# Kernel optimization log

Hardware: AMD Instinct MI355X
Metric: run time of the kernel (lower is better)

The kernel has to match this reference:

```python
import jax, jax.numpy as jnp
import numpy as np

H, D, BLK, R = 12, 64, 64, 3  # heads, size_per_head, block size, rand blocks
NEG = -1e9


def setup_inputs() -> dict:
    key = jax.random.key(0)
    ks = jax.random.split(key, 6)
    B, S, W = 2, 4096, H * D
    M = S // BLK
    return {
        "from_tensor": jax.random.normal(ks[0], (B, S, W), jnp.float32),
        "to_tensor": jax.random.normal(ks[1], (B, S, W), jnp.float32),
        "Wq": jax.random.normal(ks[2], (W, H * D), jnp.float32) * 0.02,
        "bq": jnp.zeros((H * D,), jnp.float32),
        "Wk": jax.random.normal(ks[3], (W, H * D), jnp.float32) * 0.02,
        "bk": jnp.zeros((H * D,), jnp.float32),
        "Wv": jax.random.normal(ks[4], (W, H * D), jnp.float32) * 0.02,
        "bv": jnp.zeros((H * D,), jnp.float32),
        "to_mask": jnp.ones((B, S), jnp.int32),
        "rand_attn": jax.random.randint(ks[5], (H, M - 2, R), 0, M - 2, jnp.int32),
    }


def _bigbird_block_sparse(from_tensor, to_tensor, Wq, bq, Wk, bk, Wv, bv, to_mask, rand_attn):
    B, S, _ = from_tensor.shape
    M = S // BLK
    scale = 1.0 / np.sqrt(D).astype(np.float32)

    # QKV projections -> [B,H,S,D]
    q = (from_tensor @ Wq + bq).reshape(B, S, H, D).transpose(0, 2, 1, 3)
    k = (to_tensor @ Wk + bk).reshape(B, S, H, D).transpose(0, 2, 1, 3)
    v = (to_tensor @ Wv + bv).reshape(B, S, H, D).transpose(0, 2, 1, 3)

    bq_ = q.reshape(B, H, M, BLK, D)
    bk_ = k.reshape(B, H, M, BLK, D)
    bv_ = v.reshape(B, H, M, BLK, D)

    tm = to_mask.astype(q.dtype)          # [B,S]
    bm = tm.reshape(B, M, BLK)            # [B,M,BLK]

    # gather random key/value blocks per head: [B,H,M-2,R*BLK,D]
    ha = jnp.arange(H)[:, None, None]
    gk = bk_[:, ha, rand_attn].reshape(B, H, M - 2, R * BLK, D)
    gv = bv_[:, ha, rand_attn].reshape(B, H, M - 2, R * BLK, D)
    gm = bm[:, rand_attn].reshape(B, H, M - 2, R * BLK)

    def full_row(qblk):  # first/last query blocks attend to everything
        s = jnp.einsum('bhqd,bhkd->bhqk', qblk, k) * scale + (1 - tm)[:, None, None, :] * NEG
        return jnp.einsum('bhqk,bhkd->bhqd', jax.nn.softmax(s, -1), v)

    def sparse_row(qblk, k_cat, v_cat, m_cat):  # [B,H,BLK,D] x [B,H,L,D]
        s = jnp.einsum('bhqd,bhkd->bhqk', qblk, k_cat) * scale + (1 - m_cat)[:, :, None, :] * NEG
        return jnp.einsum('bhqk,bhkd->bhqd', jax.nn.softmax(s, -1), v_cat)

    c_first = full_row(bq_[:, :, 0])
    c_last = full_row(bq_[:, :, M - 1])

    # second row: blocks [0,1,2,last] + rand
    k2 = jnp.concatenate([bk_[:, :, 0], bk_[:, :, 1], bk_[:, :, 2], bk_[:, :, M - 1], gk[:, :, 0]], axis=2)
    v2 = jnp.concatenate([bv_[:, :, 0], bv_[:, :, 1], bv_[:, :, 2], bv_[:, :, M - 1], gv[:, :, 0]], axis=2)
    m2s = jnp.concatenate([bm[:, 0], bm[:, 1], bm[:, 2], bm[:, M - 1]], axis=-1)
    m2 = jnp.concatenate([jnp.broadcast_to(m2s[:, None], (B, H, 4 * BLK)), gm[:, :, 0]], axis=-1)
    c_second = sparse_row(bq_[:, :, 1], k2, v2, m2)

    # second-to-last row: blocks [0,M-3,M-2,M-1] + rand
    k3 = jnp.concatenate([bk_[:, :, 0], bk_[:, :, M - 3], bk_[:, :, M - 2], bk_[:, :, M - 1], gk[:, :, M - 3]], axis=2)
    v3 = jnp.concatenate([bv_[:, :, 0], bv_[:, :, M - 3], bv_[:, :, M - 2], bv_[:, :, M - 1], gv[:, :, M - 3]], axis=2)
    m3s = jnp.concatenate([bm[:, 0], bm[:, M - 3], bm[:, M - 2], bm[:, M - 1]], axis=-1)
    m3 = jnp.concatenate([jnp.broadcast_to(m3s[:, None], (B, H, 4 * BLK)), gm[:, :, M - 3]], axis=-1)
    c_secondlast = sparse_row(bq_[:, :, M - 2], k3, v3, m3)

    # middle rows 2..M-3: band(prev,self,next) + rand + global first/last blocks
    L = M - 4
    band_k = jnp.concatenate([bk_[:, :, 1:M - 3], bk_[:, :, 2:M - 2], bk_[:, :, 3:M - 1]], axis=3)  # [B,H,L,3BLK,D]
    band_v = jnp.concatenate([bv_[:, :, 1:M - 3], bv_[:, :, 2:M - 2], bv_[:, :, 3:M - 1]], axis=3)
    band_m = jnp.concatenate([bm[:, 1:M - 3], bm[:, 2:M - 2], bm[:, 3:M - 1]], axis=-1)  # [B,L,3BLK]

    k_mid = jnp.concatenate([
        band_k, gk[:, :, 1:M - 3],
        jnp.broadcast_to(bk_[:, :, 0:1], (B, H, L, BLK, D)),
        jnp.broadcast_to(bk_[:, :, M - 1:M], (B, H, L, BLK, D))], axis=3)
    v_mid = jnp.concatenate([
        band_v, gv[:, :, 1:M - 3],
        jnp.broadcast_to(bv_[:, :, 0:1], (B, H, L, BLK, D)),
        jnp.broadcast_to(bv_[:, :, M - 1:M], (B, H, L, BLK, D))], axis=3)
    m_mid = jnp.concatenate([
        jnp.broadcast_to(band_m[:, None], (B, H, L, 3 * BLK)),
        gm[:, :, 1:M - 3],
        jnp.broadcast_to(bm[:, None, None, 0], (B, H, L, BLK)),
        jnp.broadcast_to(bm[:, None, None, M - 1], (B, H, L, BLK))], axis=-1)

    s_mid = jnp.einsum('bhlqd,bhlkd->bhlqk', bq_[:, :, 2:M - 2], k_mid) * scale
    s_mid = s_mid + (1 - m_mid)[:, :, :, None, :] * NEG
    c_mid = jnp.einsum('bhlqk,bhlkd->bhlqd', jax.nn.softmax(s_mid, -1), v_mid)

    ctx = jnp.concatenate([
        c_first[:, :, None], c_second[:, :, None], c_mid,
        c_secondlast[:, :, None], c_last[:, :, None]], axis=2)  # [B,H,M,BLK,D]
    return ctx.reshape(B, H, S, D).transpose(0, 2, 1, 3)  # [B,S,H,D]


def reference(from_tensor, to_tensor, Wq, bq, Wk, bk, Wv, bv, to_mask, rand_attn):
    return _bigbird_block_sparse(from_tensor, to_tensor, Wq, bq, Wk, bk, Wv, bv, to_mask, rand_attn)
```

## Files before the change

### kernel.cpp

```cpp
#include <hip/hip_runtime.h>

typedef __attribute__((ext_vector_type(4))) float f32x4;
typedef __attribute__((ext_vector_type(8))) __bf16 bf16x8;
typedef __attribute__((ext_vector_type(8))) unsigned short u16x8;
typedef __attribute__((ext_vector_type(4))) unsigned short u16x4;
typedef __attribute__((ext_vector_type(2))) unsigned int u32x2;

#define LOG2E 1.4426950408889634f

__device__ __forceinline__ unsigned short f2bf(float f) {
  unsigned u = __builtin_bit_cast(unsigned, f);
  u += 0x7fffu + ((u >> 16) & 1u);
  return (unsigned short)(u >> 16);
}

__device__ __forceinline__ unsigned cvtpk(float lo, float hi) {
  unsigned r;
  asm("v_cvt_pk_bf16_f32 %0, %1, %2" : "=v"(r) : "v"(lo), "v"(hi));
  return r;
}

__device__ __forceinline__ f32x4 mfma16(bf16x8 a, bf16x8 b, f32x4 c) {
  return __builtin_amdgcn_mfma_f32_16x16x32_bf16(a, b, c, 0, 0, 0);
}

__device__ __forceinline__ void gload_lds16(const void* g, void* l) {
  __builtin_amdgcn_global_load_lds(
      (const __attribute__((address_space(1))) void*)g,
      (__attribute__((address_space(3))) void*)l, 16, 0, 0);
}

#define NQK 6291456
#define NX 6291456
#define NW 589824

__global__ __launch_bounds__(256) void prep_kernel(
    const float* __restrict__ Wq, const float* __restrict__ Wk,
    const float* __restrict__ Wv, const float* __restrict__ from_t,
    const float* __restrict__ to_t, unsigned short* __restrict__ Wt,
    unsigned short* __restrict__ xb) {
  __shared__ float tile[64][65];
  const int bid = blockIdx.x;
  const int t = threadIdx.x;
  if (bid < 432) {
    const int z = bid / 144, rest = bid % 144;
    const float* __restrict__ src = (z == 0) ? Wq : (z == 1) ? Wk : Wv;
    unsigned short* __restrict__ dst = Wt + (size_t)z * NW;
    const int k0 = (rest / 12) * 64, n0 = (rest % 12) * 64;
    const int r = t >> 4, c4 = (t & 15) * 4;
#pragma unroll
    for (int p = 0; p < 4; ++p) {
      int rr = r + p * 16;
      f32x4 v = *(const f32x4*)(src + (size_t)(k0 + rr) * 768 + n0 + c4);
#pragma unroll
      for (int j = 0; j < 4; ++j) tile[rr][c4 + j] = v[j];
    }
    __syncthreads();
#pragma unroll
    for (int p = 0; p < 4; ++p) {
      int rn = r + p * 16;
      u16x4 o;
#pragma unroll
      for (int j = 0; j < 4; ++j) o[j] = f2bf(tile[c4 + j][rn]);
      *(u16x4*)(dst + (size_t)(n0 + rn) * 768 + k0 + c4) = o;
    }
  } else {
    const int idx = bid - 432;
    const int y = idx / 3072, xi = idx % 3072;
    const float* __restrict__ src = y ? to_t : from_t;
    unsigned short* __restrict__ dst = xb + (size_t)y * NX;
    const size_t i = ((size_t)xi * 256 + t) * 8;
    f32x4 a = *(const f32x4*)(src + i);
    f32x4 b = *(const f32x4*)(src + i + 4);
    u16x8 o;
#pragma unroll
    for (int j = 0; j < 4; ++j) { o[j] = f2bf(a[j]); o[j + 4] = f2bf(b[j]); }
    *(u16x8*)(dst + i) = o;
  }
}

__global__ __launch_bounds__(256) void qkv_gemm_kernel(
    const unsigned short* __restrict__ Xb, const unsigned short* __restrict__ Wt,
    const float* __restrict__ bq, const float* __restrict__ bk,
    const float* __restrict__ bv, unsigned short* __restrict__ qkvQK,
    unsigned short* __restrict__ vt, int zoff, int cpx) {
  __shared__ unsigned short A_lds[2][8192];
  __shared__ unsigned short B_lds[2][8192];
  const int bid0 = blockIdx.x;
  const int bid = (bid0 & 7) * cpx + (bid0 >> 3);
  const int z = zoff + bid / 384;
  const int rem = bid % 384;
  const int bm = rem / 6, bn = rem % 6;
  const unsigned short* __restrict__ X = Xb + (z ? (size_t)NX : 0);
  const unsigned short* __restrict__ Wz = Wt + (size_t)z * NW;
  const float* __restrict__ bias = (z == 0) ? bq : (z == 1) ? bk : bv;
  const int t = threadIdx.x, lane = t & 63, w = t >> 6;
  const int wm = (w >> 1) * 64, wn = (w & 1) * 64;
  const int l15 = lane & 15, cc = lane >> 4;

  f32x4 acc[4][4];
#pragma unroll
  for (int i = 0; i < 4; ++i)
#pragma unroll
    for (int j = 0; j < 4; ++j) acc[i][j] = (f32x4){0.f, 0.f, 0.f, 0.f};

  const unsigned short* Abase = X + (size_t)bm * 128 * 768;
  const unsigned short* Bbase = Wz + (size_t)bn * 128 * 768;

  auto STAGE = [&](int ks, int bufi) {
#pragma unroll
    for (int p = 0; p < 4; ++p) {
      int wb = p * 4 + w;
      int ch = wb * 64 + lane;
      int r = ch >> 3, sl = ch & 7;
      int g = sl ^ (r & 7);
      gload_lds16(Abase + (size_t)r * 768 + ks * 64 + g * 8,
                  &A_lds[bufi][wb * 512]);
      gload_lds16(Bbase + (size_t)r * 768 + ks * 64 + g * 8,
                  &B_lds[bufi][wb * 512]);
    }
  };

  STAGE(0, 0);

  for (int ks = 0; ks < 12; ++ks) {
    const int cur = ks & 1;
    if (ks < 11) {
      STAGE(ks + 1, cur ^ 1);
      asm volatile("s_waitcnt vmcnt(8)" ::: "memory");
    } else {
      asm volatile("s_waitcnt vmcnt(0)" ::: "memory");
    }
    __builtin_amdgcn_s_barrier();
    __builtin_amdgcn_sched_barrier(0);

    bf16x8 af[4][2], bfr[4][2];
#pragma unroll
    for (int mi = 0; mi < 4; ++mi) {
      int row = wm + mi * 16 + l15;
      const char* rp = (const char*)A_lds[cur] + row * 128;
#pragma unroll
      for (int kk = 0; kk < 2; ++kk)
        af[mi][kk] = *(const bf16x8*)(rp + (((cc + 4 * kk) ^ (row & 7)) << 4));
    }
#pragma unroll
    for (int ni = 0; ni < 4; ++ni) {
      int row = wn + ni * 16 + l15;
      const char* rp = (const char*)B_lds[cur] + row * 128;
#pragma unroll
      for (int kk = 0; kk < 2; ++kk)
        bfr[ni][kk] = *(const bf16x8*)(rp + (((cc + 4 * kk) ^ (row & 7)) << 4));
    }
#pragma unroll
    for (int kk = 0; kk < 2; ++kk)
#pragma unroll
      for (int mi = 0; mi < 4; ++mi)
#pragma unroll
        for (int ni = 0; ni < 4; ++ni)
          acc[mi][ni] = mfma16(af[mi][kk], bfr[ni][kk], acc[mi][ni]);
    asm volatile("s_waitcnt lgkmcnt(0)" ::: "memory");
    __builtin_amdgcn_s_barrier();
  }

  if (z < 2) {
    const float qscale = (z == 0) ? 0.125f * LOG2E : 1.0f;
    unsigned short* __restrict__ dst = qkvQK + (size_t)z * NQK;
#pragma unroll
    for (int ni = 0; ni < 4; ++ni) {
      int gn = bn * 128 + wn + ni * 16 + l15;
      float bv_ = bias[gn];
      int hh = gn >> 6, dd = gn & 63;
#pragma unroll
      for (int mi = 0; mi < 4; ++mi) {
#pragma unroll
        for (int r = 0; r < 4; ++r) {
          int gm = bm * 128 + wm + mi * 16 + cc * 4 + r;
          int bb = gm >> 12, s = gm & 4095;
          float val = (acc[mi][ni][r] + bv_) * qscale;
          dst[((((size_t)bb * 12 + hh) * 4096 + s) * 64) + dd] = f2bf(val);
        }
      }
    }
  } else {
#pragma unroll
    for (int ni = 0; ni < 4; ++ni) {
      int gn = bn * 128 + wn + ni * 16 + l15;
      float bv_ = bias[gn];
      int hh = gn >> 6, dd = gn & 63;
#pragma unroll
      for (int mi = 0; mi < 4; ++mi) {
        int gm0 = bm * 128 + wm + mi * 16 + cc * 4;
        int bb = gm0 >> 12, s0 = gm0 & 4095;
        u16x4 o;
#pragma unroll
        for (int r = 0; r < 4; ++r) o[r] = f2bf(acc[mi][ni][r] + bv_);
        *(u16x4*)(vt + ((size_t)(bb * 12 + hh) * 64 + dd) * 4096 + s0) = o;
      }
    }
  }
}

__global__ __launch_bounds__(256) void attn_kernel(
    const unsigned short* __restrict__ qkvQK, const unsigned short* __restrict__ vt,
    const int* __restrict__ to_mask, const int* __restrict__ rand_attn,
    float* __restrict__ out, float* __restrict__ part_o,
    float* __restrict__ part_ml) {
  __shared__ unsigned short K_lds[4][4096];
  __shared__ unsigned short VT_lds[4][4096];
  __shared__ unsigned short P_lds[4][1024];
  __shared__ float penal[8][64];
  __shared__ int blist[8];

  const int bid0 = blockIdx.x;
  const int bid = (bid0 & 7) * 234 + (bid0 >> 3);
  const int bh = bid / 78, r78 = bid % 78;
  const int h = bh % 12, b = bh / 12;
  const int t = threadIdx.x, lane = t & 63, w = t >> 6;
  const int l15 = lane & 15, cc = lane >> 4;

  int m, nblk, chunk = 0;
  bool full;
  if (r78 < 62) {
    full = false;
    m = r78 + 1;
    nblk = (m == 1 || m == 62) ? 7 : 8;
    if (t == 0) {
      const int* rp = rand_attn + ((size_t)h * 62 + (m - 1)) * 3;
      if (m == 1) {
        blist[0] = 0; blist[1] = 1; blist[2] = 2; blist[3] = 63;
        blist[4] = rp[0]; blist[5] = rp[1]; blist[6] = rp[2];
      } else if (m == 62) {
        blist[0] = 0; blist[1] = 61; blist[2] = 62; blist[3] = 63;
        blist[4] = rp[0]; blist[5] = rp[1]; blist[6] = rp[2];
      } else {
        blist[0] = m - 1; blist[1] = m; blist[2] = m + 1;
        blist[3] = rp[0]; blist[4] = rp[1]; blist[5] = rp[2];
        blist[6] = 0; blist[7] = 63;
      }
    }
  } else {
    full = true;
    int fr = r78 - 62;
    chunk = fr & 7;
    m = (fr >> 3) ? 63 : 0;
    nblk = 8;
    if (t < 8) blist[t] = chunk * 8 + t;
  }

  const unsigned short* qp = qkvQK + (((size_t)b * 12 + h) * 4096 + m * 64) * 64;
  const unsigned short* kp = qkvQK + NQK + (((size_t)b * 12 + h) * 4096) * 64;
  const unsigned short* vtp = vt + (((size_t)b * 12 + h) * 64) * 4096;

  int loff[2];
  const unsigned short *kpl[2], *vpl[2];
#pragma unroll
  for (int p = 0; p < 2; ++p) {
    int wb = p * 4 + w;
    int ch = wb * 64 + lane;
    int rr = ch >> 3;
    int g = (ch & 7) ^ (rr & 7);
    loff[p] = wb * 512;
    kpl[p] = kp + rr * 64 + g * 8;
    vpl[p] = vtp + rr * 4096 + g * 8;
  }

  bf16x8 aq[2];
  {
    int qrow = w * 16 + l15;
    aq[0] = *(const bf16x8*)(qp + qrow * 64 + cc * 8);
    aq[1] = *(const bf16x8*)(qp + qrow * 64 + 32 + cc * 8);
  }

  float m_run = -INFINITY, l_run = 0.f;
  f32x4 o_acc[4];
#pragma unroll
  for (int dg = 0; dg < 4; ++dg) o_acc[dg] = (f32x4){0.f, 0.f, 0.f, 0.f};

  char* pw = (char*)P_lds[w];
  const int swz = (l15 & 7) << 4;

  auto STAGE = [&](int kb, int bufi) {
    const size_t ko = (size_t)kb * 4096;
    const size_t vo = (size_t)kb * 64;
    gload_lds16(kpl[0] + ko, &K_lds[bufi][loff[0]]);
    gload_lds16(kpl[1] + ko, &K_lds[bufi][loff[1]]);
    gload_lds16(vpl[0] + vo, &VT_lds[bufi][loff[0]]);
    gload_lds16(vpl[1] + vo, &VT_lds[bufi][loff[1]]);
  };

  __syncthreads();

  {
    int ib = w;
#pragma unroll
    for (int pp = 0; pp < 2; ++pp, ib += 4)
      if (ib < nblk)
        penal[ib][lane] =
            (1.0f - (float)to_mask[(size_t)b * 4096 + blist[ib] * 64 + lane]) *
            (-1e9f * LOG2E);
  }
  STAGE(blist[0], 0);
  STAGE(blist[1], 1);
  asm volatile("s_waitcnt lgkmcnt(0)" ::: "memory");
  __builtin_amdgcn_s_barrier();

  for (int ib = 0; ib < nblk; ++ib) {
    const int bi = ib & 3;
    if (ib + 2 < nblk) {
      STAGE(blist[ib + 2], (ib + 2) & 3);
      asm volatile("s_waitcnt vmcnt(8)" ::: "memory");
    } else if (ib + 1 < nblk) {
      asm volatile("s_waitcnt vmcnt(4)" ::: "memory");
    } else {
      asm volatile("s_waitcnt vmcnt(0)" ::: "memory");
    }
    __builtin_amdgcn_s_barrier();
    __builtin_amdgcn_sched_barrier(0);

    float sm[4][4];
    const char* kbase = (const char*)K_lds[bi];
#pragma unroll
    for (int kg = 0; kg < 4; ++kg) {
      int krow = kg * 16 + l15;
      const char* rp = kbase + krow * 128;
      int sz = (krow & 7) << 4;
      bf16x8 k0 = *(const bf16x8*)(rp + ((cc << 4) ^ sz));
      bf16x8 k1 = *(const bf16x8*)(rp + (((cc + 4) << 4) ^ sz));
      f32x4 zz = (f32x4){0.f, 0.f, 0.f, 0.f};
      zz = mfma16(k0, aq[0], zz);
      zz = mfma16(k1, aq[1], zz);
      f32x4 pen = *(const f32x4*)(&penal[ib][kg * 16 + cc * 4]);
#pragma unroll
      for (int r = 0; r < 4; ++r) sm[kg][r] = zz[r] + pen[r];
    }

    float mk[4];
#pragma unroll
    for (int kg = 0; kg < 4; ++kg)
      mk[kg] = fmaxf(fmaxf(sm[kg][0], sm[kg][1]), fmaxf(sm[kg][2], sm[kg][3]));
    float mx = fmaxf(fmaxf(mk[0], mk[1]), fmaxf(mk[2], mk[3]));
    mx = fmaxf(mx, __shfl_xor(mx, 16, 64));
    mx = fmaxf(mx, __shfl_xor(mx, 32, 64));

    if (!__all(mx - m_run <= 8.0f)) {
      float mn = fmaxf(m_run, mx);
      float fac = exp2f(m_run - mn);
      m_run = mn;
      l_run *= fac;
      float fr_[4];
#pragma unroll
      for (int r = 0; r < 4; ++r) fr_[r] = __shfl(fac, cc * 4 + r, 64);
#pragma unroll
      for (int dg = 0; dg < 4; ++dg)
#pragma unroll
        for (int r = 0; r < 4; ++r) o_acc[dg][r] *= fr_[r];
    }

    float rs = 0.f;
#pragma unroll
    for (int kg = 0; kg < 4; ++kg) {
      float p0 = exp2f(sm[kg][0] - m_run), p1 = exp2f(sm[kg][1] - m_run);
      float p2 = exp2f(sm[kg][2] - m_run), p3 = exp2f(sm[kg][3] - m_run);
      rs += (p0 + p1) + (p2 + p3);
      u32x2 wv;
      wv[0] = cvtpk(p0, p1);
      wv[1] = cvtpk(p2, p3);
      *(u32x2*)(pw + l15 * 128 + ((kg * 32 + cc * 8) ^ swz)) = wv;
    }
    rs += __shfl_xor(rs, 16, 64);
    rs += __shfl_xor(rs, 32, 64);
    l_run += rs;

    __builtin_amdgcn_wave_barrier();
    bf16x8 ap0 = *(const bf16x8*)(pw + l15 * 128 + ((cc << 4) ^ swz));
    bf16x8 ap1 = *(const bf16x8*)(pw + l15 * 128 + (((cc + 4) << 4) ^ swz));

    const char* vbase = (const char*)VT_lds[bi];
#pragma unroll
    for (int dg = 0; dg < 4; ++dg) {
      int drow = dg * 16 + l15;
      const char* vb = vbase + drow * 128;
      int sz = (drow & 7) << 4;
      bf16x8 v0 = *(const bf16x8*)(vb + ((cc << 4) ^ sz));
      bf16x8 v1 = *(const bf16x8*)(vb + (((cc + 4) << 4) ^ sz));
      o_acc[dg] = mfma16(ap0, v0, o_acc[dg]);
      o_acc[dg] = mfma16(ap1, v1, o_acc[dg]);
    }
  }

  if (!full) {
    float inv[4];
#pragma unroll
    for (int r = 0; r < 4; ++r) inv[r] = 1.0f / __shfl(l_run, cc * 4 + r, 64);
#pragma unroll
    for (int r = 0; r < 4; ++r) {
      int s = m * 64 + w * 16 + cc * 4 + r;
#pragma unroll
      for (int dg = 0; dg < 4; ++dg) {
        int d = dg * 16 + l15;
        out[(((size_t)b * 4096 + s) * 12 + h) * 64 + d] = o_acc[dg][r] * inv[r];
      }
    }
  } else {
    const int row = (b * 12 + h) * 2 + (m ? 1 : 0);
    float* po = part_o + (((size_t)row * 8 + chunk) * 64) * 64;
    float* pml = part_ml + ((size_t)row * 8 + chunk) * 128;
#pragma unroll
    for (int r = 0; r < 4; ++r) {
      int q = w * 16 + cc * 4 + r;
#pragma unroll
      for (int dg = 0; dg < 4; ++dg) {
        int d = dg * 16 + l15;
        po[q * 64 + d] = o_acc[dg][r];
      }
    }
    if (cc == 0) {
      pml[w * 16 + l15] = m_run;
      pml[64 + w * 16 + l15] = l_run;
    }
  }
}

__global__ __launch_bounds__(256) void combine_kernel(
    const float* __restrict__ part_o, const float* __restrict__ part_ml,
    float* __restrict__ out) {
  const int row = blockIdx.x;
  const int b = row / 24, h = (row >> 1) % 12, m = (row & 1) ? 63 : 0;
  const int t = threadIdx.x;
  const int q = t >> 2, d0 = (t & 3) * 16;

  float mc[8], lc[8];
  float M = -INFINITY;
#pragma unroll
  for (int c = 0; c < 8; ++c) {
    const float* pml = part_ml + ((size_t)row * 8 + c) * 128;
    mc[c] = pml[q];
    lc[c] = pml[64 + q];
    M = fmaxf(M, mc[c]);
  }
  float wgt[8], L = 0.f;
#pragma unroll
  for (int c = 0; c < 8; ++c) {
    wgt[c] = exp2f(mc[c] - M);
    L += wgt[c] * lc[c];
  }
  f32x4 acc[4];
#pragma unroll
  for (int j = 0; j < 4; ++j) acc[j] = (f32x4){0.f, 0.f, 0.f, 0.f};
#pragma unroll
  for (int c = 0; c < 8; ++c) {
    const float* po = part_o + (((size_t)row * 8 + c) * 64 + q) * 64 + d0;
#pragma unroll
    for (int j = 0; j < 4; ++j) {
      f32x4 v = *(const f32x4*)(po + j * 4);
#pragma unroll
      for (int e = 0; e < 4; ++e) acc[j][e] += wgt[c] * v[e];
    }
  }
  const float inv = 1.0f / L;
  const int s = m * 64 + q;
  float* op = out + (((size_t)b * 4096 + s) * 12 + h) * 64 + d0;
#pragma unroll
  for (int j = 0; j < 4; ++j) {
    f32x4 v;
#pragma unroll
    for (int e = 0; e < 4; ++e) v[e] = acc[j][e] * inv;
    *(f32x4*)(op + j * 4) = v;
  }
}

extern "C" void kernel_launch(void* const* d_in, const int* in_sizes, int n_in,
                              void* d_out, int out_size, void* d_ws,
                              size_t ws_size, hipStream_t stream) {
  (void)in_sizes; (void)n_in; (void)out_size;
  const float* from_t = (const float*)d_in[0];
  const float* to_t = (const float*)d_in[1];
  const float* Wq = (const float*)d_in[2];
  const float* bq = (const float*)d_in[3];
  const float* Wk = (const float*)d_in[4];
  const float* bk = (const float*)d_in[5];
  const float* Wv = (const float*)d_in[6];
  const float* bv = (const float*)d_in[7];
  const int* to_mask = (const int*)d_in[8];
  const int* rand_attn = (const int*)d_in[9];
  float* out = (float*)d_out;

  unsigned short* Wt = (unsigned short*)d_ws;
  unsigned short* qkvQK = Wt + (size_t)3 * NW;
  unsigned short* Xb = qkvQK + (size_t)2 * NQK;

  const size_t part_elems = (size_t)48 * 8 * 64 * 64 + (size_t)48 * 8 * 128;
  const size_t fused_bytes =
      ((size_t)3 * NW + 2 * NQK + 2 * NX + NQK) * 2 + part_elems * 4;

  if (ws_size >= fused_bytes) {
    unsigned short* vt = Xb + (size_t)2 * NX;
    float* part_o = (float*)Xb;
    float* part_ml = part_o + (size_t)48 * 8 * 64 * 64;

    prep_kernel<<<dim3(6576), dim3(256), 0, stream>>>(Wq, Wk, Wv, from_t, to_t,
                                                      Wt, Xb);
    qkv_gemm_kernel<<<dim3(1152), dim3(256), 0, stream>>>(
        Xb, Wt, bq, bk, bv, qkvQK, vt, 0, 144);
    attn_kernel<<<dim3(1872), dim3(256), 0, stream>>>(
        qkvQK, vt, to_mask, rand_attn, out, part_o, part_ml);
    combine_kernel<<<dim3(48), dim3(256), 0, stream>>>(part_o, part_ml, out);
  } else {
    unsigned short* vt = Xb;
    float* part_o = (float*)(Xb + (size_t)NX);
    float* part_ml = part_o + (size_t)48 * 8 * 64 * 64;

    prep_kernel<<<dim3(6576), dim3(256), 0, stream>>>(Wq, Wk, Wv, from_t, to_t,
                                                      Wt, Xb);
    qkv_gemm_kernel<<<dim3(768), dim3(256), 0, stream>>>(
        Xb, Wt, bq, bk, bv, qkvQK, vt, 0, 96);
    qkv_gemm_kernel<<<dim3(384), dim3(256), 0, stream>>>(
        Xb, Wt, bq, bk, bv, qkvQK, vt, 2, 48);
    attn_kernel<<<dim3(1872), dim3(256), 0, stream>>>(
        qkvQK, vt, to_mask, rand_attn, out, part_o, part_ml);
    combine_kernel<<<dim3(48), dim3(256), 0, stream>>>(part_o, part_ml, out);
  }
}
```

Before: 116.7 us.

## Software-pipeline QK of next block with softmax/PV of current and halve LDS buffers

The attention loop now computes the QK^T scores for block ib+1 before the softmax and PV work of block ib, so matrix-core work overlaps with the exp/max VALU work. K and V loads are staged separately: K runs two blocks ahead and V one block ahead. This lets the K and V LDS buffers shrink from four to two slots, which cuts LDS use and may raise occupancy. s_setprio is raised around the MFMA sections. The cost is a full vmcnt(0) wait each iteration and extra registers for the second score tile.

```diff
diff --git a/kernel.cpp b/kernel.cpp
--- a/kernel.cpp
+++ b/kernel.cpp
@@ -205,8 +205,8 @@
     const int* __restrict__ to_mask, const int* __restrict__ rand_attn,
     float* __restrict__ out, float* __restrict__ part_o,
     float* __restrict__ part_ml) {
-  __shared__ unsigned short K_lds[4][4096];
-  __shared__ unsigned short VT_lds[4][4096];
+  __shared__ unsigned short K_lds[2][4096];
+  __shared__ unsigned short VT_lds[2][4096];
   __shared__ unsigned short P_lds[4][1024];
   __shared__ float penal[8][64];
   __shared__ int blist[8];
@@ -279,46 +279,20 @@
   char* pw = (char*)P_lds[w];
   const int swz = (l15 & 7) << 4;
 
-  auto STAGE = [&](int kb, int bufi) {
+  auto STAGE_K = [&](int kb, int bufi) {
     const size_t ko = (size_t)kb * 4096;
-    const size_t vo = (size_t)kb * 64;
     gload_lds16(kpl[0] + ko, &K_lds[bufi][loff[0]]);
     gload_lds16(kpl[1] + ko, &K_lds[bufi][loff[1]]);
+  };
+  auto STAGE_V = [&](int kb, int bufi) {
+    const size_t vo = (size_t)kb * 64;
     gload_lds16(vpl[0] + vo, &VT_lds[bufi][loff[0]]);
     gload_lds16(vpl[1] + vo, &VT_lds[bufi][loff[1]]);
   };
 
-  __syncthreads();
-
-  {
-    int ib = w;
-#pragma unroll
-    for (int pp = 0; pp < 2; ++pp, ib += 4)
-      if (ib < nblk)
-        penal[ib][lane] =
-            (1.0f - (float)to_mask[(size_t)b * 4096 + blist[ib] * 64 + lane]) *
-            (-1e9f * LOG2E);
-  }
-  STAGE(blist[0], 0);
-  STAGE(blist[1], 1);
-  asm volatile("s_waitcnt lgkmcnt(0)" ::: "memory");
-  __builtin_amdgcn_s_barrier();
-
-  for (int ib = 0; ib < nblk; ++ib) {
-    const int bi = ib & 3;
-    if (ib + 2 < nblk) {
-      STAGE(blist[ib + 2], (ib + 2) & 3);
-      asm volatile("s_waitcnt vmcnt(8)" ::: "memory");
-    } else if (ib + 1 < nblk) {
-      asm volatile("s_waitcnt vmcnt(4)" ::: "memory");
-    } else {
-      asm volatile("s_waitcnt vmcnt(0)" ::: "memory");
-    }
-    __builtin_amdgcn_s_barrier();
-    __builtin_amdgcn_sched_barrier(0);
-
-    float sm[4][4];
-    const char* kbase = (const char*)K_lds[bi];
+  auto QK = [&](int bufi, int slot, float s[4][4]) {
+    const char* kbase = (const char*)K_lds[bufi];
+    __builtin_amdgcn_s_setprio(1);
 #pragma unroll
     for (int kg = 0; kg < 4; ++kg) {
       int krow = kg * 16 + l15;
@@ -329,10 +303,44 @@
       f32x4 zz = (f32x4){0.f, 0.f, 0.f, 0.f};
       zz = mfma16(k0, aq[0], zz);
       zz = mfma16(k1, aq[1], zz);
-      f32x4 pen = *(const f32x4*)(&penal[ib][kg * 16 + cc * 4]);
-#pragma unroll
-      for (int r = 0; r < 4; ++r) sm[kg][r] = zz[r] + pen[r];
-    }
+      f32x4 pen = *(const f32x4*)(&penal[slot][kg * 16 + cc * 4]);
+#pragma unroll
+      for (int r = 0; r < 4; ++r) s[kg][r] = zz[r] + pen[r];
+    }
+    __builtin_amdgcn_s_setprio(0);
+  };
+
+  __syncthreads();
+
+  {
+    int ib = w;
+#pragma unroll
+    for (int pp = 0; pp < 2; ++pp, ib += 4)
+      if (ib < nblk)
+        penal[ib][lane] =
+            (1.0f - (float)to_mask[(size_t)b * 4096 + blist[ib] * 64 + lane]) *
+            (-1e9f * LOG2E);
+  }
+  STAGE_K(blist[0], 0);
+  STAGE_V(blist[0], 0);
+  STAGE_K(blist[1], 1);
+  asm volatile("s_waitcnt vmcnt(4) lgkmcnt(0)" ::: "memory");
+  __builtin_amdgcn_s_barrier();
+  __builtin_amdgcn_sched_barrier(0);
+
+  float sm[4][4];
+  QK(0, 0, sm);
+
+  for (int ib = 0; ib < nblk; ++ib) {
+    asm volatile("s_waitcnt vmcnt(0)" ::: "memory");
+    __builtin_amdgcn_s_barrier();
+    __builtin_amdgcn_sched_barrier(0);
+
+    if (ib + 2 < nblk) STAGE_K(blist[ib + 2], ib & 1);
+    if (ib + 1 < nblk) STAGE_V(blist[ib + 1], (ib + 1) & 1);
+
+    float sn[4][4];
+    if (ib + 1 < nblk) QK((ib + 1) & 1, ib + 1, sn);
 
     float mk[4];
 #pragma unroll
@@ -375,7 +383,8 @@
     bf16x8 ap0 = *(const bf16x8*)(pw + l15 * 128 + ((cc << 4) ^ swz));
     bf16x8 ap1 = *(const bf16x8*)(pw + l15 * 128 + (((cc + 4) << 4) ^ swz));
 
-    const char* vbase = (const char*)VT_lds[bi];
+    const char* vbase = (const char*)VT_lds[ib & 1];
+    __builtin_amdgcn_s_setprio(1);
 #pragma unroll
     for (int dg = 0; dg < 4; ++dg) {
       int drow = dg * 16 + l15;
@@ -385,6 +394,14 @@
       bf16x8 v1 = *(const bf16x8*)(vb + (((cc + 4) << 4) ^ sz));
       o_acc[dg] = mfma16(ap0, v0, o_acc[dg]);
       o_acc[dg] = mfma16(ap1, v1, o_acc[dg]);
+    }
+    __builtin_amdgcn_s_setprio(0);
+
+    if (ib + 1 < nblk) {
+#pragma unroll
+      for (int kg = 0; kg < 4; ++kg)
+#pragma unroll
+        for (int r = 0; r < 4; ++r) sm[kg][r] = sn[kg][r];
     }
   }
 
```

Result: faster. 109.6 us (-6.0%).
